# Kernel tuning notes

Measured on AMD Instinct MI355X. Metric: run time of the kernel, lower is better.

Reference implementation:

```python
import jax, jax.numpy as jnp
import numpy as np

B, L, NS, EPS = 512, 20, 16, 32   # sessions, seq_len, nodes/session, edges/session
H, V, STEP = 128, 100000, 1       # hidden, vocab (n_node), ggnn layers


def _xavier(key, shape):
    fan_out, fan_in = shape[0], shape[1]
    a = float(np.sqrt(6.0 / (fan_in + fan_out)))
    return jax.random.uniform(key, shape, minval=-a, maxval=a, dtype=jnp.float32)


def setup_inputs() -> dict:
    key = jax.random.key(0)
    ks = jax.random.split(key, 20)
    # node item ids per session (nonzero)
    items = jax.random.randint(ks[0], (B, NS), 1, V)
    # intra-session edges, offset to global node indices
    src_l = jax.random.randint(ks[1], (B, EPS), 0, NS)
    dst_l = jax.random.randint(ks[2], (B, EPS), 0, NS)
    offs = (jnp.arange(B) * NS)[:, None]
    edge_index = jnp.stack([(src_l + offs).reshape(-1), (dst_l + offs).reshape(-1)])
    # sequences drawn from each session's own nodes, padded with 0
    seq_pos = jax.random.randint(ks[3], (B, L), 0, NS)
    lengths = jax.random.randint(ks[4], (B,), 5, L + 1)
    mask = (jnp.arange(L)[None, :] < lengths[:, None]).astype(jnp.int32)
    sequence = jnp.where(mask == 1, jnp.take_along_axis(items, seq_pos, axis=1), 0)

    stdv = 1.0 / float(np.sqrt(H))
    embedding = jax.random.uniform(ks[5], (V, H), minval=-stdv, maxval=stdv, dtype=jnp.float32)
    embedding = embedding.at[0].set(0.0)  # padding_idx=0
    ggnn_w = _xavier(ks[6], (STEP * H, H)).reshape(STEP, H, H)
    W_ih = _xavier(ks[7], (3 * H, H))
    W_hh = _xavier(ks[8], (3 * H, H))
    b_ih = jnp.zeros((3 * H,), jnp.float32)
    b_hh = jnp.zeros((3 * H,), jnp.float32)
    W1 = _xavier(ks[9], (H, H)); b1 = jnp.zeros((H,), jnp.float32)
    W2 = _xavier(ks[10], (H, H)); b2 = jnp.zeros((H,), jnp.float32)
    w3 = _xavier(ks[11], (1, H))
    Wt = _xavier(ks[12], (H, 2 * H)); bt = jnp.zeros((H,), jnp.float32)
    gamma = jnp.ones((H,), jnp.float32); beta = jnp.zeros((H,), jnp.float32)
    return dict(items=items, edge_index=edge_index, sequence=sequence, mask=mask,
                embedding=embedding, ggnn_w=ggnn_w, W_ih=W_ih, W_hh=W_hh,
                b_ih=b_ih, b_hh=b_hh, W1=W1, b1=b1, W2=W2, b2=b2, w3=w3,
                Wt=Wt, bt=bt, gamma=gamma, beta=beta)


def reference(items, edge_index, sequence, mask, embedding, ggnn_w, W_ih, W_hh,
              b_ih, b_hh, W1, b1, W2, b2, w3, Wt, bt, gamma, beta):
    N = B * NS
    x = embedding[items.reshape(-1)]               # [N, H] node features
    src, dst = edge_index[0], edge_index[1]
    # GatedGraphConv: per-layer linear, scatter-add aggregation, GRUCell update
    for l in range(STEP):
        m = x @ ggnn_w[l]                          # [N, H]
        agg = jax.ops.segment_sum(m[src], dst, num_segments=N)
        gi = agg @ W_ih.T + b_ih                   # [N, 3H]
        gh = x @ W_hh.T + b_hh
        ir, iz, inn = jnp.split(gi, 3, axis=-1)
        hr, hz, hn = jnp.split(gh, 3, axis=-1)
        r = jax.nn.sigmoid(ir + hr)
        z = jax.nn.sigmoid(iz + hz)
        n = jnp.tanh(inn + r * hn)
        x = (1.0 - z) * n + z * x
    xg = x.reshape(B, NS, H)
    # ragged gather: for each seq position, first node whose item id matches
    match = sequence[:, :, None] == items[:, None, :]      # [B, L, NS]
    has = match.any(-1)
    idx = jnp.argmax(match, axis=-1)                       # first match
    gathered = jnp.take_along_axis(xg, idx[..., None], axis=1)  # [B, L, H]
    fallback = embedding[sequence]                         # item not in graph
    hidden = jnp.where(has[..., None], gathered, fallback)
    hidden = jnp.where((sequence == 0)[..., None], 0.0, hidden)
    # compute_scores: attention pooling + hybrid transform + layernorm
    seq_lens = mask.sum(axis=1) - 1
    ht = hidden[jnp.arange(B), seq_lens]                   # [B, H] last item
    q1 = (ht @ W1.T + b1)[:, None, :]                      # [B, 1, H]
    q2 = hidden @ W2.T + b2                                # [B, L, H]
    alpha = jax.nn.sigmoid(q1 + q2) @ w3.T                 # [B, L, 1]
    mf = mask[..., None].astype(hidden.dtype)
    a = jnp.sum(alpha * hidden * mf, axis=1)               # [B, H]
    a = jnp.concatenate([a, ht], axis=1) @ Wt.T + bt       # hybrid (nonhybrid=False)
    mu = a.mean(-1, keepdims=True)
    var = ((a - mu) ** 2).mean(-1, keepdims=True)
    a = (a - mu) / jnp.sqrt(var + 1e-5) * gamma + beta
    scores = a @ embedding[1:].T                           # [B, V-1]
    return scores
```

## Files before the change

kernel.cpp:

```cpp
#include <hip/hip_runtime.h>
#include <hip/hip_bf16.h>
#include <hip/hip_fp16.h>

#define B_ 512
#define L_ 20
#define NS_ 16
#define EPS_ 32
#define H_ 128
#define V_ 100000
#define N_NODES (B_*NS_)
#define N_EDGES (B_*EPS_)
#define NV (V_-1)

typedef _Float16 half8 __attribute__((ext_vector_type(8)));
typedef float floatx4 __attribute__((ext_vector_type(4)));

#define PITCH 136

__global__ void k_prep(const int* __restrict__ items, const float* __restrict__ emb,
                       const float* __restrict__ Wg, const float* __restrict__ Whh,
                       const float* __restrict__ Wih, const float* __restrict__ W2,
                       const float* __restrict__ W1,
                       float* __restrict__ x, _Float16* __restrict__ WgT_h,
                       _Float16* __restrict__ Whh_h, _Float16* __restrict__ Wih_h,
                       _Float16* __restrict__ W2_h, _Float16* __restrict__ W1_h) {
  int i = blockIdx.x*256 + threadIdx.x;
  if (i < N_NODES*H_) {
    int n = i >> 7, h = i & 127;
    x[i] = emb[(size_t)items[n]*H_ + h];
    return;
  }
  i -= N_NODES*H_;
  if (i < H_*H_) { int j = i>>7, k = i&127; WgT_h[i] = (_Float16)Wg[k*H_ + j]; return; }
  i -= H_*H_;
  if (i < 3*H_*H_) { Whh_h[i] = (_Float16)Whh[i]; return; }
  i -= 3*H_*H_;
  if (i < 3*H_*H_) { Wih_h[i] = (_Float16)Wih[i]; return; }
  i -= 3*H_*H_;
  if (i < H_*H_) { W2_h[i] = (_Float16)W2[i]; return; }
  i -= H_*H_;
  if (i < H_*H_) { W1_h[i] = (_Float16)W1[i]; return; }
}

__global__ __launch_bounds__(256) void k_gemm128(
    const float* __restrict__ A, const _Float16* __restrict__ B0,
    const _Float16* __restrict__ B1, int switch_mt,
    float* __restrict__ C, int N) {
  __shared__ _Float16 lds_a[64*PITCH];
  __shared__ _Float16 lds_b[64*PITCH];
  const int tid = threadIdx.x;
  const int mt = blockIdx.y, nt = blockIdx.x;
  const _Float16* __restrict__ Bp = (mt < switch_mt) ? B0 : B1;
  #pragma unroll
  for (int i = 0; i < 8; i++) {
    int lin = i*256 + tid;
    int row = lin >> 5, c4 = lin & 31;
    const float4 v = *reinterpret_cast<const float4*>(&A[(size_t)(mt*64+row)*H_ + c4*4]);
    union { _Float16 h[4]; uint2 u; } p;
    p.h[0]=(_Float16)v.x; p.h[1]=(_Float16)v.y; p.h[2]=(_Float16)v.z; p.h[3]=(_Float16)v.w;
    *reinterpret_cast<uint2*>(&lds_a[row*PITCH + c4*4]) = p.u;
  }
  #pragma unroll
  for (int i = 0; i < 4; i++) {
    int lin = i*256 + tid;
    int row = lin >> 4, ch = lin & 15;
    uint4 v = *reinterpret_cast<const uint4*>(&Bp[(size_t)(nt*64+row)*H_ + ch*8]);
    *reinterpret_cast<uint4*>(&lds_b[row*PITCH + ch*8]) = v;
  }
  __syncthreads();
  const int w = tid >> 6, lane = tid & 63, quad = lane >> 4, r16 = lane & 15;
  half8 afr[4];
  #pragma unroll
  for (int kk = 0; kk < 4; kk++)
    afr[kk] = *reinterpret_cast<const half8*>(&lds_a[(w*16 + r16)*PITCH + kk*32 + quad*8]);
  floatx4 acc[4];
  #pragma unroll
  for (int n4 = 0; n4 < 4; n4++) acc[n4] = (floatx4){0.f,0.f,0.f,0.f};
  #pragma unroll
  for (int n4 = 0; n4 < 4; n4++) {
    #pragma unroll
    for (int kk = 0; kk < 4; kk++) {
      half8 bfr = *reinterpret_cast<const half8*>(&lds_b[(n4*16 + r16)*PITCH + kk*32 + quad*8]);
      acc[n4] = __builtin_amdgcn_mfma_f32_16x16x32_f16(afr[kk], bfr, acc[n4], 0, 0, 0);
    }
  }
  #pragma unroll
  for (int n4 = 0; n4 < 4; n4++)
    #pragma unroll
    for (int r = 0; r < 4; r++) {
      int row = mt*64 + w*16 + quad*4 + r;
      int col = nt*64 + n4*16 + r16;
      C[(size_t)row*N + col] = acc[n4][r];
    }
}

__global__ __launch_bounds__(128) void k_scatter(const int* __restrict__ edge_index,
                                                 const float* __restrict__ mgh,
                                                 float* __restrict__ agg) {
  __shared__ float acc[NS_*H_];
  const int b = blockIdx.x, h = threadIdx.x;
  #pragma unroll
  for (int j = 0; j < NS_; j++) acc[j*H_ + h] = 0.f;
  for (int e = 0; e < EPS_; e++) {
    int se = edge_index[b*EPS_ + e];
    int de = edge_index[N_EDGES + b*EPS_ + e];
    acc[(de - b*NS_)*H_ + h] += mgh[(size_t)se*512 + h];
  }
  #pragma unroll
  for (int j = 0; j < NS_; j++) agg[(size_t)(b*NS_ + j)*H_ + h] = acc[j*H_ + h];
}

__global__ void k_gru(const float* __restrict__ gi, const float* __restrict__ mgh,
                      const float* __restrict__ b_ih, const float* __restrict__ b_hh,
                      float* __restrict__ x) {
  int i = blockIdx.x*256 + threadIdx.x;
  int n = i >> 7, h = i & 127;
  float ir  = gi[(size_t)n*384 + h]        + b_ih[h];
  float iz  = gi[(size_t)n*384 + 128 + h]  + b_ih[128 + h];
  float in_ = gi[(size_t)n*384 + 256 + h]  + b_ih[256 + h];
  float hr  = mgh[(size_t)n*512 + 128 + h] + b_hh[h];
  float hz  = mgh[(size_t)n*512 + 256 + h] + b_hh[128 + h];
  float hn  = mgh[(size_t)n*512 + 384 + h] + b_hh[256 + h];
  float r = 1.f/(1.f + __expf(-(ir + hr)));
  float z = 1.f/(1.f + __expf(-(iz + hz)));
  float nn = tanhf(in_ + r*hn);
  x[i] = (1.f - z)*nn + z*x[i];
}

__global__ void k_hidden(const int* __restrict__ items, const int* __restrict__ sequence,
                         const int* __restrict__ mask, const float* __restrict__ xg,
                         const float* __restrict__ emb, float* __restrict__ Hbuf) {
  int tid = threadIdx.x;
  int r = blockIdx.x*2 + (tid >> 7);
  int h = tid & 127;
  int b, l;
  if (r < B_*L_) { b = r / L_; l = r - b*L_; }
  else {
    b = r - B_*L_;
    int len = 0;
    for (int i = 0; i < L_; i++) len += mask[b*L_ + i];
    l = len - 1;
  }
  int seqv = sequence[b*L_ + l];
  float val = 0.f;
  if (seqv != 0) {
    int idx = -1;
    #pragma unroll
    for (int j = 0; j < NS_; j++) { if (idx < 0 && items[b*NS_ + j] == seqv) idx = j; }
    val = (idx >= 0) ? xg[(size_t)(b*NS_ + idx)*H_ + h] : emb[(size_t)seqv*H_ + h];
  }
  Hbuf[(size_t)r*H_ + h] = val;
}

__global__ __launch_bounds__(128) void k_attn(
    const float* __restrict__ Hbuf, const float* __restrict__ q,
    const float* __restrict__ b1, const float* __restrict__ b2,
    const float* __restrict__ w3, const float* __restrict__ Wt,
    const float* __restrict__ bt, const float* __restrict__ gamma,
    const float* __restrict__ beta, _Float16* __restrict__ a_h) {
  __shared__ float red[2];
  __shared__ float cat[256];
  const int b = blockIdx.x, t = threadIdx.x;
  float q1b = q[(size_t)(B_*L_ + b)*H_ + t] + b1[t] + b2[t];
  float w3t = w3[t];
  float at = 0.f;
  for (int l = 0; l < L_; l++) {
    float s = q1b + q[(size_t)(b*L_ + l)*H_ + t];
    float v = (1.f/(1.f + __expf(-s))) * w3t;
    #pragma unroll
    for (int o = 32; o > 0; o >>= 1) v += __shfl_down(v, o);
    if ((t & 63) == 0) red[t >> 6] = v;
    __syncthreads();
    float alpha = red[0] + red[1];
    __syncthreads();
    at += alpha * Hbuf[(size_t)(b*L_ + l)*H_ + t];
  }
  float htv = Hbuf[(size_t)(B_*L_ + b)*H_ + t];
  cat[t] = at; cat[128 + t] = htv;
  __syncthreads();
  float hyb = bt[t];
  const float* wrow = &Wt[(size_t)t*256];
  #pragma unroll 4
  for (int k = 0; k < 256; k++) hyb += cat[k]*wrow[k];
  float s = hyb;
  #pragma unroll
  for (int o = 32; o > 0; o >>= 1) s += __shfl_down(s, o);
  if ((t & 63) == 0) red[t >> 6] = s;
  __syncthreads();
  float mu = (red[0] + red[1]) * (1.f/128.f);
  __syncthreads();
  float d = hyb - mu;
  float s2 = d*d;
  #pragma unroll
  for (int o = 32; o > 0; o >>= 1) s2 += __shfl_down(s2, o);
  if ((t & 63) == 0) red[t >> 6] = s2;
  __syncthreads();
  float var = (red[0] + red[1]) * (1.f/128.f);
  float y = d * rsqrtf(var + 1e-5f) * gamma[t] + beta[t];
  a_h[(size_t)b*H_ + t] = (_Float16)y;
}

__global__ __launch_bounds__(256) void k_scores(
    const _Float16* __restrict__ a_h, const float* __restrict__ emb,
    float* __restrict__ out) {
  __shared__ _Float16 lds_a[128*PITCH];
  __shared__ _Float16 lds_b[64*PITCH];
  const int tid = threadIdx.x;
  const int nt = blockIdx.x, mg = blockIdx.y;
  #pragma unroll
  for (int i = 0; i < 8; i++) {
    int lin = i*256 + tid;
    int row = lin >> 4, ch = lin & 15;
    uint4 v = *reinterpret_cast<const uint4*>(&a_h[(size_t)(mg*128 + row)*H_ + ch*8]);
    *reinterpret_cast<uint4*>(&lds_a[row*PITCH + ch*8]) = v;
  }
  #pragma unroll
  for (int i = 0; i < 8; i++) {
    int lin = i*256 + tid;
    int row = lin >> 5, c4 = lin & 31;
    int g = nt*64 + row;
    float4 v = {0.f, 0.f, 0.f, 0.f};
    if (g < NV) v = *reinterpret_cast<const float4*>(&emb[(size_t)(1 + g)*H_ + c4*4]);
    union { _Float16 h[4]; uint2 u; } p;
    p.h[0]=(_Float16)v.x; p.h[1]=(_Float16)v.y; p.h[2]=(_Float16)v.z; p.h[3]=(_Float16)v.w;
    *reinterpret_cast<uint2*>(&lds_b[row*PITCH + c4*4]) = p.u;
  }
  __syncthreads();
  const int w = tid >> 6, lane = tid & 63, quad = lane >> 4, r16 = lane & 15;
  half8 afr[2][4];
  #pragma unroll
  for (int ms = 0; ms < 2; ms++)
    #pragma unroll
    for (int kk = 0; kk < 4; kk++)
      afr[ms][kk] = *reinterpret_cast<const half8*>(&lds_a[(w*32 + ms*16 + r16)*PITCH + kk*32 + quad*8]);
  floatx4 acc[2][4];
  #pragma unroll
  for (int ms = 0; ms < 2; ms++)
    #pragma unroll
    for (int n4 = 0; n4 < 4; n4++) acc[ms][n4] = (floatx4){0.f,0.f,0.f,0.f};
  #pragma unroll
  for (int n4 = 0; n4 < 4; n4++) {
    #pragma unroll
    for (int kk = 0; kk < 4; kk++) {
      half8 bfr = *reinterpret_cast<const half8*>(&lds_b[(n4*16 + r16)*PITCH + kk*32 + quad*8]);
      acc[0][n4] = __builtin_amdgcn_mfma_f32_16x16x32_f16(afr[0][kk], bfr, acc[0][n4], 0, 0, 0);
      acc[1][n4] = __builtin_amdgcn_mfma_f32_16x16x32_f16(afr[1][kk], bfr, acc[1][n4], 0, 0, 0);
    }
  }
  #pragma unroll
  for (int ms = 0; ms < 2; ms++)
    #pragma unroll
    for (int n4 = 0; n4 < 4; n4++)
      #pragma unroll
      for (int r = 0; r < 4; r++) {
        int row = mg*128 + w*32 + ms*16 + quad*4 + r;
        int col = nt*64 + n4*16 + r16;
        if (col < NV) out[(size_t)row*NV + col] = acc[ms][n4][r];
      }
}

extern "C" void kernel_launch(void* const* d_in, const int* in_sizes, int n_in,
                              void* d_out, int out_size, void* d_ws, size_t ws_size,
                              hipStream_t stream) {
  const int*   items     = (const int*)d_in[0];
  const int*   edge_index= (const int*)d_in[1];
  const int*   sequence  = (const int*)d_in[2];
  const int*   mask      = (const int*)d_in[3];
  const float* emb       = (const float*)d_in[4];
  const float* ggnn_w    = (const float*)d_in[5];
  const float* W_ih      = (const float*)d_in[6];
  const float* W_hh      = (const float*)d_in[7];
  const float* b_ih      = (const float*)d_in[8];
  const float* b_hh      = (const float*)d_in[9];
  const float* W1        = (const float*)d_in[10];
  const float* b1        = (const float*)d_in[11];
  const float* W2        = (const float*)d_in[12];
  const float* b2        = (const float*)d_in[13];
  const float* w3        = (const float*)d_in[14];
  const float* Wt        = (const float*)d_in[15];
  const float* bt        = (const float*)d_in[16];
  const float* gamma     = (const float*)d_in[17];
  const float* beta      = (const float*)d_in[18];

  char* ws = (char*)d_ws;
  float* x    = (float*)(ws + 0);
  float* mgh  = (float*)(ws + 4194304);
  float* q    = (float*)(ws + 4194304);
  float* agg  = (float*)(ws + 20971520);
  float* Hbuf = (float*)(ws + 20971520);
  float* gi   = (float*)(ws + 26476544);
  _Float16* a_h   = (_Float16*)(ws + 39059456);
  _Float16* WgT_h = (_Float16*)(ws + 39190528);
  _Float16* Whh_h = (_Float16*)(ws + 39223296);
  _Float16* Wih_h = (_Float16*)(ws + 39321600);
  _Float16* W2_h  = (_Float16*)(ws + 39419904);
  _Float16* W1_h  = (_Float16*)(ws + 39452672);
  float* out = (float*)d_out;

  k_prep<<<4672, 256, 0, stream>>>(items, emb, ggnn_w, W_hh, W_ih, W2, W1,
                                   x, WgT_h, Whh_h, Wih_h, W2_h, W1_h);
  k_gemm128<<<dim3(8, 128), 256, 0, stream>>>(x, WgT_h, WgT_h, 1 << 30, mgh, 512);
  k_scatter<<<512, 128, 0, stream>>>(edge_index, mgh, agg);
  k_gemm128<<<dim3(6, 128), 256, 0, stream>>>(agg, Wih_h, Wih_h, 1 << 30, gi, 384);
  k_gru<<<4096, 256, 0, stream>>>(gi, mgh, b_ih, b_hh, x);
  k_hidden<<<5376, 256, 0, stream>>>(items, sequence, mask, x, emb, Hbuf);
  k_gemm128<<<dim3(2, 168), 256, 0, stream>>>(Hbuf, W2_h, W1_h, 160, q, 128);
  k_attn<<<512, 128, 0, stream>>>(Hbuf, q, b1, b2, w3, Wt, bt, gamma, beta, a_h);
  k_scores<<<dim3(1563, 4), 256, 0, stream>>>(a_h, emb, out);
}
```

Measured before the change: 430.2 us.

## Fuse scatter, input GEMM and GRU into one per-session kernel; remap score grid

Replaces the edge scatter, the W_ih GEMM and the GRU update kernels with a single per-session kernel. It aggregates messages in LDS, runs the 16x384 MFMA product against W_ih directly from global memory, and applies the GRU gates from LDS, which removes the agg and gi round trips and two launches. The scores kernel now uses a flattened 1D grid where consecutive blocks cover the 4 batch groups of 8 adjacent embedding tiles, so each embedding tile is reused from cache by all four groups. Trade-offs: the fused kernel has low parallelism (512 blocks, 128 threads idle during the scatter), and the scores grid now launches padded blocks that exit early.

```diff
diff --git a/kernel.cpp b/kernel.cpp
--- a/kernel.cpp
+++ b/kernel.cpp
@@ -94,37 +94,70 @@
     }
 }
 
-__global__ __launch_bounds__(128) void k_scatter(const int* __restrict__ edge_index,
-                                                 const float* __restrict__ mgh,
-                                                 float* __restrict__ agg) {
-  __shared__ float acc[NS_*H_];
-  const int b = blockIdx.x, h = threadIdx.x;
-  #pragma unroll
-  for (int j = 0; j < NS_; j++) acc[j*H_ + h] = 0.f;
-  for (int e = 0; e < EPS_; e++) {
-    int se = edge_index[b*EPS_ + e];
-    int de = edge_index[N_EDGES + b*EPS_ + e];
-    acc[(de - b*NS_)*H_ + h] += mgh[(size_t)se*512 + h];
-  }
-  #pragma unroll
-  for (int j = 0; j < NS_; j++) agg[(size_t)(b*NS_ + j)*H_ + h] = acc[j*H_ + h];
-}
-
-__global__ void k_gru(const float* __restrict__ gi, const float* __restrict__ mgh,
-                      const float* __restrict__ b_ih, const float* __restrict__ b_hh,
-                      float* __restrict__ x) {
-  int i = blockIdx.x*256 + threadIdx.x;
-  int n = i >> 7, h = i & 127;
-  float ir  = gi[(size_t)n*384 + h]        + b_ih[h];
-  float iz  = gi[(size_t)n*384 + 128 + h]  + b_ih[128 + h];
-  float in_ = gi[(size_t)n*384 + 256 + h]  + b_ih[256 + h];
-  float hr  = mgh[(size_t)n*512 + 128 + h] + b_hh[h];
-  float hz  = mgh[(size_t)n*512 + 256 + h] + b_hh[128 + h];
-  float hn  = mgh[(size_t)n*512 + 384 + h] + b_hh[256 + h];
-  float r = 1.f/(1.f + __expf(-(ir + hr)));
-  float z = 1.f/(1.f + __expf(-(iz + hz)));
-  float nn = tanhf(in_ + r*hn);
-  x[i] = (1.f - z)*nn + z*x[i];
+#define GILP 385
+__global__ __launch_bounds__(256) void k_gnn(
+    const int* __restrict__ edge_index, const float* __restrict__ mgh,
+    const _Float16* __restrict__ Wih, const float* __restrict__ b_ih,
+    const float* __restrict__ b_hh, float* __restrict__ x) {
+  __shared__ __align__(16) _Float16 a16[NS_*PITCH];
+  __shared__ __align__(16) float gil[NS_*GILP];
+  float* agg = gil;
+  const int b = blockIdx.x, tid = threadIdx.x;
+  if (tid < 128) {
+    #pragma unroll
+    for (int j = 0; j < NS_; j++) agg[j*128 + tid] = 0.f;
+    for (int e = 0; e < EPS_; e++) {
+      int se = edge_index[b*EPS_ + e];
+      int de = edge_index[N_EDGES + b*EPS_ + e] - b*NS_;
+      agg[de*128 + tid] += mgh[(size_t)se*512 + tid];
+    }
+  }
+  __syncthreads();
+  #pragma unroll
+  for (int j = 0; j < 8; j++) {
+    int idx = j*256 + tid;
+    a16[(idx >> 7)*PITCH + (idx & 127)] = (_Float16)agg[idx];
+  }
+  __syncthreads();
+  const int w = tid >> 6, lane = tid & 63, quad = lane >> 4, r16 = lane & 15;
+  half8 afr[4];
+  #pragma unroll
+  for (int kk = 0; kk < 4; kk++)
+    afr[kk] = *reinterpret_cast<const half8*>(&a16[r16*PITCH + kk*32 + quad*8]);
+  floatx4 acc[6];
+  #pragma unroll
+  for (int t = 0; t < 6; t++) acc[t] = (floatx4){0.f,0.f,0.f,0.f};
+  #pragma unroll
+  for (int t = 0; t < 6; t++) {
+    int g = w*6 + t;
+    #pragma unroll
+    for (int kk = 0; kk < 4; kk++) {
+      half8 bfr = *reinterpret_cast<const half8*>(&Wih[(size_t)(g*16 + r16)*H_ + kk*32 + quad*8]);
+      acc[t] = __builtin_amdgcn_mfma_f32_16x16x32_f16(afr[kk], bfr, acc[t], 0, 0, 0);
+    }
+  }
+  #pragma unroll
+  for (int t = 0; t < 6; t++)
+    #pragma unroll
+    for (int r = 0; r < 4; r++)
+      gil[(quad*4 + r)*GILP + (w*6 + t)*16 + r16] = acc[t][r];
+  __syncthreads();
+  #pragma unroll
+  for (int j = 0; j < 8; j++) {
+    int idx = j*256 + tid;
+    int nl = idx >> 7, h = idx & 127;
+    size_t node = (size_t)b*NS_ + nl;
+    float ir  = gil[nl*GILP + h]       + b_ih[h];
+    float iz  = gil[nl*GILP + 128 + h] + b_ih[128 + h];
+    float in_ = gil[nl*GILP + 256 + h] + b_ih[256 + h];
+    float hr  = mgh[node*512 + 128 + h] + b_hh[h];
+    float hz  = mgh[node*512 + 256 + h] + b_hh[128 + h];
+    float hn  = mgh[node*512 + 384 + h] + b_hh[256 + h];
+    float rr = 1.f/(1.f + __expf(-(ir + hr)));
+    float zz = 1.f/(1.f + __expf(-(iz + hz)));
+    float nn = tanhf(in_ + rr*hn);
+    x[node*H_ + h] = (1.f - zz)*nn + zz*x[node*H_ + h];
+  }
 }
 
 __global__ void k_hidden(const int* __restrict__ items, const int* __restrict__ sequence,
@@ -206,7 +239,10 @@
   __shared__ _Float16 lds_a[128*PITCH];
   __shared__ _Float16 lds_b[64*PITCH];
   const int tid = threadIdx.x;
-  const int nt = blockIdx.x, mg = blockIdx.y;
+  const int d = blockIdx.x;
+  const int nt = (d >> 5)*8 + (d & 7);
+  const int mg = (d >> 3) & 3;
+  if (nt >= 1563) return;
   #pragma unroll
   for (int i = 0; i < 8; i++) {
     int lin = i*256 + tid;
@@ -286,9 +322,7 @@
   float* x    = (float*)(ws + 0);
   float* mgh  = (float*)(ws + 4194304);
   float* q    = (float*)(ws + 4194304);
-  float* agg  = (float*)(ws + 20971520);
   float* Hbuf = (float*)(ws + 20971520);
-  float* gi   = (float*)(ws + 26476544);
   _Float16* a_h   = (_Float16*)(ws + 39059456);
   _Float16* WgT_h = (_Float16*)(ws + 39190528);
   _Float16* Whh_h = (_Float16*)(ws + 39223296);
@@ -300,11 +334,9 @@
   k_prep<<<4672, 256, 0, stream>>>(items, emb, ggnn_w, W_hh, W_ih, W2, W1,
                                    x, WgT_h, Whh_h, Wih_h, W2_h, W1_h);
   k_gemm128<<<dim3(8, 128), 256, 0, stream>>>(x, WgT_h, WgT_h, 1 << 30, mgh, 512);
-  k_scatter<<<512, 128, 0, stream>>>(edge_index, mgh, agg);
-  k_gemm128<<<dim3(6, 128), 256, 0, stream>>>(agg, Wih_h, Wih_h, 1 << 30, gi, 384);
-  k_gru<<<4096, 256, 0, stream>>>(gi, mgh, b_ih, b_hh, x);
+  k_gnn<<<512, 256, 0, stream>>>(edge_index, mgh, Wih_h, b_ih, b_hh, x);
   k_hidden<<<5376, 256, 0, stream>>>(items, sequence, mask, x, emb, Hbuf);
   k_gemm128<<<dim3(2, 168), 256, 0, stream>>>(Hbuf, W2_h, W1_h, 160, q, 128);
   k_attn<<<512, 128, 0, stream>>>(Hbuf, q, b1, b2, w3, Wt, bt, gamma, beta, a_h);
-  k_scores<<<dim3(1563, 4), 256, 0, stream>>>(a_h, emb, out);
-}
+  k_scores<<<6272, 256, 0, stream>>>(a_h, emb, out);
+}
```

Result: slower. 449.4 us (+4.5%).
